# Performance work log

Hardware: AMD Instinct MI355X
Metric: run time of the kernel (lower is better)

## Reference

```python
import jax, jax.numpy as jnp
import numpy as np

CLB, CUB = 0.0, 255.0
SHORTCUT = (True, False, False, False, False)  # formatInput2Tuple((True,False), bool, 5, strict=False)


def _pad_same(kh, kw):
    kch, kcw = (kh + 1) // 2, (kw + 1) // 2
    return (kch - 1, kh - kch, kcw - 1, kw - kcw)


def _sym_pad(x, p):
    return jnp.pad(x, ((0, 0), (0, 0), (p[0], p[1]), (p[2], p[3])), mode='symmetric')


def _psf2otf(psf, shape):
    kh, kw = psf.shape[-2], psf.shape[-1]
    z = jnp.zeros(psf.shape[:-2] + shape, psf.dtype)
    z = z.at[..., :kh, :kw].set(psf)
    z = jnp.roll(z, (-(kh // 2), -(kw // 2)), axis=(-2, -1))
    return jnp.fft.fft2(z)


def _wnorm(w, scale):
    # zero-mean + L2 normalize per output filter, then learned per-filter scale
    wz = w - w.mean(axis=(-3, -2, -1), keepdims=True)
    n = jnp.sqrt((wz * wz).sum(axis=(-3, -2, -1), keepdims=True))
    return wz / n * scale[..., None, None, None]


def _conv2d(x, w, pad):
    return jax.lax.conv_general_dilated(_sym_pad(x, pad), w, (1, 1), 'VALID',
                                        dimension_numbers=('NCHW', 'OIHW', 'NCHW'))


def _convT2d(x, w, pad):
    # adjoint of VALID correlation, then crop by pad (nconv_transpose2D)
    kh, kw = w.shape[-2], w.shape[-1]
    wt = jnp.flip(w, (-2, -1)).transpose(1, 0, 2, 3)
    y = jax.lax.conv_general_dilated(x, wt, (1, 1), [(kh - 1, kh - 1), (kw - 1, kw - 1)],
                                     dimension_numbers=('NCHW', 'OIHW', 'NCHW'))
    return y[:, :, pad[0]:y.shape[2] - pad[1], pad[2]:y.shape[3] - pad[3]]


def _prelu(x, a):
    return jnp.where(x >= 0, x, a[None, :, None, None] * x)


def _edgetaper(x, psf):
    # MATLAB-style edgetaper: blend image with its circular blur near borders
    H, W = x.shape[-2], x.shape[-1]

    def a1(p, n):
        z = jnp.fft.ifft(jnp.abs(jnp.fft.fft(p, n - 1)) ** 2).real
        z = jnp.concatenate([z, z[:1]])
        return 1.0 - z / z.max()

    ah = a1(psf.sum(1), H)
    aw = a1(psf.sum(0), W)
    alpha = ah[:, None] * aw[None, :]
    otf = _psf2otf(psf, (H, W))
    blurred = jnp.fft.ifft2(jnp.fft.fft2(x) * otf[None, None]).real
    return alpha * x + (1.0 - alpha) * blurred


def _forward(x, blur_kernel, stdn, wiener_w, wiener_scale, alpha, conv_w, scale_f,
             bias_f, bias_t, rpa_prelu1, rpa_w1, rpa_scale1, rpa_b1,
             rpa_prelu2, rpa_w2, rpa_scale2, rpa_b2, alpha_proj, mix_weights):
    kh, kw = blur_kernel.shape
    pw = _pad_same(kh, kw)
    xp = _sym_pad(x, pw)
    xp = _edgetaper(xp, blur_kernel)
    B, C, Hp, Wp = xp.shape
    D = alpha.shape[0]

    # ---- multi-Wiener deconvolution in the Fourier domain ----
    ww = _wnorm(wiener_w, wiener_scale)                 # (F, wC, kh, kw)
    Hf = _psf2otf(blur_kernel, (Hp, Wp))                # (Hp, Wp) complex
    Gf = _psf2otf(ww, (Hp, Wp))                         # (F, wC, Hp, Wp)
    S = (jnp.abs(Gf) ** 2).sum(0)                       # (wC, Hp, Wp), wC=1 shared over channels
    Y = jnp.fft.fft2(xp)                                # (B, C, Hp, Wp)
    a = jnp.exp(alpha)                                  # (D, 1)
    denom = (jnp.abs(Hf) ** 2)[None, None] + a[:, :, None, None] * S[None]  # (D, C, Hp, Wp)
    T = jnp.conj(Hf)[None, None] / denom                # Wiener transfer functions
    xw = jnp.fft.ifft2(T[None] * Y[:, None]).real       # (B, D, C, Hp, Wp)
    amp = (jnp.abs(T) ** 2).mean(axis=(-2, -1))         # (D, C) noise amplification
    cstdn = jnp.sqrt(stdn[:, None] ** 2 * amp.mean(-1)[None])  # (B, D)
    cstdn = cstdn.reshape(-1)                           # (B*D,)

    z = xw.reshape(B * D, C, Hp, Wp)

    # ---- feature conv + residual pre-activation stack ----
    pc = _pad_same(conv_w.shape[-2], conv_w.shape[-1])
    cw = _wnorm(conv_w, scale_f)
    out = _conv2d(z, cw, pc) + bias_f[None, :, None, None]

    pr = _pad_same(rpa_w1.shape[-2], rpa_w1.shape[-1])
    for i in range(rpa_w1.shape[0]):
        t = _prelu(out, rpa_prelu1[i])
        t = _conv2d(t, _wnorm(rpa_w1[i], rpa_scale1[i]), pr) + rpa_b1[i][None, :, None, None]
        t = _prelu(t, rpa_prelu2[i])
        t = _conv2d(t, _wnorm(rpa_w2[i], rpa_scale2[i]), pr) + rpa_b2[i][None, :, None, None]
        out = out + t if SHORTCUT[i] else t

    out = _convT2d(out, cw, pc) + bias_t[None, :, None, None]

    # ---- L2 ball projection ----
    N = C * Hp * Wp
    eps = jnp.exp(alpha_proj[0]) * cstdn * np.float32(np.sqrt(N - 1))
    nrm = jnp.sqrt((out * out).sum(axis=(1, 2, 3)))
    scl = jnp.where(nrm > eps, eps / jnp.maximum(nrm, 1e-12), 1.0)
    out = out * scl[:, None, None, None]

    # ---- residual, box projection, crop, weighted mix over Wiener branches ----
    res = jnp.clip(z - out, CLB, CUB)
    res = res[:, :, pw[0]:Hp - pw[1], pw[2]:Wp - pw[3]]
    res = res.reshape(B, D, C, res.shape[-2], res.shape[-1])
    return (res * mix_weights).sum(axis=1)


def setup_inputs():
    key = jax.random.key(0)
    ks = jax.random.split(key, 8)
    B, C, H, W = 2, 1, 256, 256
    Dp = 5
    x = jax.random.uniform(ks[0], (B, C, H, W), jnp.float32) * 255.0
    bk = jax.random.uniform(ks[1], (15, 15), jnp.float32) + 1e-3
    bk = bk / bk.sum()
    stdn = jax.random.uniform(ks[2], (B,), jnp.float32) * 9.0 + 1.0
    return {
        'x': x,
        'blur_kernel': bk,
        'stdn': stdn,
        'wiener_w': jax.random.normal(ks[3], (24, 1, 5, 5), jnp.float32),
        'wiener_scale': jnp.full((24,), 0.1, jnp.float32),
        'alpha': jnp.log(jnp.logspace(np.log10(1e-3), np.log10(0.1), 4))[:, None].astype(jnp.float32),
        'conv_w': jax.random.normal(ks[4], (32, 1, 5, 5), jnp.float32),
        'scale_f': jnp.ones((32,), jnp.float32),
        'bias_f': jnp.zeros((32,), jnp.float32),
        'bias_t': jnp.zeros((1,), jnp.float32),
        'rpa_prelu1': jnp.full((Dp, 32), 0.1, jnp.float32),
        'rpa_w1': jax.random.normal(ks[5], (Dp, 64, 32, 3, 3), jnp.float32),
        'rpa_scale1': jnp.ones((Dp, 64), jnp.float32),
        'rpa_b1': jnp.zeros((Dp, 64), jnp.float32),
        'rpa_prelu2': jnp.full((Dp, 64), 0.1, jnp.float32),
        'rpa_w2': jax.random.normal(ks[6], (Dp, 32, 64, 3, 3), jnp.float32),
        'rpa_scale2': jnp.ones((Dp, 32), jnp.float32),
        'rpa_b2': jnp.zeros((Dp, 32), jnp.float32),
        'alpha_proj': jnp.zeros((1,), jnp.float32),
        'mix_weights': jnp.full((1, 4, 1, 1, 1), 0.25, jnp.float32),
    }


def reference(x, blur_kernel, stdn, wiener_w, wiener_scale, alpha, conv_w, scale_f,
              bias_f, bias_t, rpa_prelu1, rpa_w1, rpa_scale1, rpa_b1,
              rpa_prelu2, rpa_w2, rpa_scale2, rpa_b2, alpha_proj, mix_weights):
    return _forward(x, blur_kernel, stdn, wiener_w, wiener_scale, alpha, conv_w, scale_f,
                    bias_f, bias_t, rpa_prelu1, rpa_w1, rpa_scale1, rpa_b1,
                    rpa_prelu2, rpa_w2, rpa_scale2, rpa_b2, alpha_proj, mix_weights)
```

## Files before the change

### kernel.cpp

```cpp
#include <hip/hip_runtime.h>
#include <math.h>

#define HP     270
#define PLANE  72900
#define PW     272
#define PPLANE 73984

typedef unsigned int uint32;
typedef unsigned short ushort;
typedef __attribute__((ext_vector_type(8))) short bf16x8;
typedef __attribute__((ext_vector_type(4))) float f32x4;

__device__ __forceinline__ float blockReduceSum(float val) {
  __shared__ float sh[16];
  int lane = threadIdx.x & 63, wid = threadIdx.x >> 6;
#pragma unroll
  for (int o = 32; o > 0; o >>= 1) val += __shfl_down(val, o, 64);
  __syncthreads();
  if (lane == 0) sh[wid] = val;
  __syncthreads();
  float tot = 0.f;
  int nw = (blockDim.x + 63) >> 6;
  for (int i = 0; i < nw; ++i) tot += sh[i];
  return tot;
}

__global__ __launch_bounds__(256) void k_twiddle(float2* __restrict__ tw) {
  int idx = blockIdx.x * 256 + threadIdx.x;
  if (idx >= PLANE) return;
  int j = idx / HP, k = idx % HP;
  int m = (j * k) % HP;
  double ang = (2.0 * M_PI * (double)m) / 270.0;
  tw[idx] = make_float2((float)cos(ang), (float)sin(ang));
}

__global__ __launch_bounds__(256) void k_sympad(const float* __restrict__ x, float* __restrict__ xp) {
  int idx = blockIdx.x * 256 + threadIdx.x;
  if (idx >= 2 * PLANE) return;
  int b = idx / PLANE, p = idx % PLANE;
  int i = p / HP, j = p % HP;
  int si = i - 7; si = si < 0 ? -1 - si : (si > 255 ? 511 - si : si);
  int sj = j - 7; sj = sj < 0 ? -1 - sj : (sj > 255 ? 511 - sj : sj);
  xp[idx] = x[(b * 256 + si) * 256 + sj];
}

__global__ __launch_bounds__(512) void k_edget(const float* __restrict__ bk, float* __restrict__ ahw) {
  __shared__ float pr[15], pc[15], acr[15], accl[15];
  int t = threadIdx.x;
  if (t < 15) {
    float sr = 0.f, scv = 0.f;
    for (int k = 0; k < 15; ++k) { sr += bk[t * 15 + k]; scv += bk[k * 15 + t]; }
    pr[t] = sr; pc[t] = scv;
  }
  __syncthreads();
  if (t < 30) {
    int l = t % 15; bool isr = (t < 15);
    const float* p = isr ? pr : pc;
    float s = 0.f;
    for (int j = 0; j + l < 15; ++j) s += p[j] * p[j + l];
    if (isr) acr[l] = s; else accl[l] = s;
  }
  __syncthreads();
  for (int i = t; i < 540; i += blockDim.x) {
    bool isr = (i < 270);
    int ii = isr ? i : i - 270;
    const float* ac = isr ? acr : accl;
    int m = (ii == 269) ? 0 : ii;
    float zv;
    if (m < 15) zv = ac[m];
    else if (m >= 255) zv = ac[269 - m];
    else zv = 0.f;
    ahw[i] = 1.f - zv / ac[0];
  }
}

__global__ __launch_bounds__(256) void k_Hf(const float* __restrict__ bk, float2* __restrict__ Hf) {
  int p = blockIdx.x * 256 + threadIdx.x;
  if (p >= PLANE) return;
  int u = p / HP, v = p % HP;
  float2 er[15], es[15];
#pragma unroll
  for (int r = 0; r < 15; ++r) {
    int m = ((u * (r - 7)) % HP + HP) % HP;
    float sn, cs;
    sincosf(2.f * (float)M_PI * (float)m / 270.f, &sn, &cs);
    er[r] = make_float2(cs, -sn);
    int m2 = ((v * (r - 7)) % HP + HP) % HP;
    sincosf(2.f * (float)M_PI * (float)m2 / 270.f, &sn, &cs);
    es[r] = make_float2(cs, -sn);
  }
  float ar = 0.f, ai = 0.f;
#pragma unroll 1
  for (int r = 0; r < 15; ++r) {
    float rr = 0.f, ri = 0.f;
#pragma unroll
    for (int s = 0; s < 15; ++s) {
      float wv = bk[r * 15 + s];
      rr += wv * es[s].x; ri += wv * es[s].y;
    }
    ar += er[r].x * rr - er[r].y * ri;
    ai += er[r].x * ri + er[r].y * rr;
  }
  Hf[p] = make_float2(ar, ai);
}

__global__ __launch_bounds__(256) void k_wnorm(const float* __restrict__ w, const float* __restrict__ scale,
                                               float* __restrict__ out, int fsize) {
  int f = blockIdx.x;
  const float* wf = w + (size_t)f * fsize;
  float s = 0.f;
  for (int i = threadIdx.x; i < fsize; i += 256) s += wf[i];
  float mean = blockReduceSum(s) / (float)fsize;
  float s2 = 0.f;
  for (int i = threadIdx.x; i < fsize; i += 256) { float d = wf[i] - mean; s2 += d * d; }
  float nrm = sqrtf(blockReduceSum(s2));
  float sc = scale[f] / nrm;
  for (int i = threadIdx.x; i < fsize; i += 256) out[(size_t)f * fsize + i] = (wf[i] - mean) * sc;
}

__global__ void k_wT(const float* __restrict__ cwn, float* __restrict__ wT) {
  int idx = blockIdx.x * 256 + threadIdx.x;
  if (idx >= 800) return;
  int t = idx >> 5, f = idx & 31;
  int dri = t / 5, dci = t % 5;
  wT[t * 32 + f] = cwn[f * 25 + (4 - dri) * 5 + (4 - dci)];
}

template <int CIN, int COUT>
__global__ __launch_bounds__(256) void k_wfrag(const float* __restrict__ w, const float* __restrict__ scale,
                                               unsigned short* __restrict__ outb) {
  constexpr int KC = CIN / 32, MT = COUT / 16, FS = CIN * 9;
  int fg = blockIdx.x;
  int f = fg % COUT, iter = fg / COUT;
  const float* wf = w + (size_t)fg * FS;
  float s = 0.f;
  for (int i = threadIdx.x; i < FS; i += 256) s += wf[i];
  float mean = blockReduceSum(s) / (float)FS;
  float s2 = 0.f;
  for (int i = threadIdx.x; i < FS; i += 256) { float d = wf[i] - mean; s2 += d * d; }
  float nrm = sqrtf(blockReduceSum(s2));
  float scv = scale[fg] / nrm;
  unsigned short* dst0 = outb + (size_t)iter * (9 * KC * MT * 64 * 16);
  for (int i = threadIdx.x; i < FS; i += 256) {
    float val = (wf[i] - mean) * scv;
    int ci = i / 9, rs = i - ci * 9;
    int kc = ci >> 5, cil = ci & 31, q = cil >> 3, j = cil & 7;
    int mt = f >> 4, ocl = f & 15, lane = q * 16 + ocl;
    unsigned short* d2 = dst0 + ((((rs * KC + kc) * MT + mt) * 64 + lane) * 16);
    uint32 u = __float_as_uint(val);
    d2[j] = (unsigned short)(u >> 16);
    float lof = val - __uint_as_float(u & 0xFFFF0000u);
    d2[8 + j] = (unsigned short)(__float_as_uint(lof) >> 16);
  }
}

__global__ __launch_bounds__(256) void k_S(const float* __restrict__ wwn, float* __restrict__ S) {
  int p = blockIdx.x * 256 + threadIdx.x;
  if (p >= PLANE) return;
  int u = p / HP, v = p % HP;
  float2 er[5], es[5];
#pragma unroll
  for (int r = 0; r < 5; ++r) {
    float sn, cs;
    int m = (u * r) % HP;
    sincosf(2.f * (float)M_PI * (float)m / 270.f, &sn, &cs);
    er[r] = make_float2(cs, -sn);
    int m2 = (v * r) % HP;
    sincosf(2.f * (float)M_PI * (float)m2 / 270.f, &sn, &cs);
    es[r] = make_float2(cs, -sn);
  }
  float prr[25], pii[25];
#pragma unroll
  for (int r = 0; r < 5; ++r)
#pragma unroll
    for (int s = 0; s < 5; ++s) {
      prr[r * 5 + s] = er[r].x * es[s].x - er[r].y * es[s].y;
      pii[r * 5 + s] = er[r].x * es[s].y + er[r].y * es[s].x;
    }
  float acc = 0.f;
#pragma unroll 1
  for (int f = 0; f < 24; ++f) {
    float xr = 0.f, xi = 0.f;
#pragma unroll
    for (int t = 0; t < 25; ++t) {
      float wv = wwn[f * 25 + t];
      xr += wv * prr[t]; xi += wv * pii[t];
    }
    acc += xr * xr + xi * xi;
  }
  S[p] = acc;
}

__global__ __launch_bounds__(256) void k_T(const float2* __restrict__ Hf, const float* __restrict__ S,
                                           const float* __restrict__ alpha, float2* __restrict__ T) {
  int idx = blockIdx.x * 256 + threadIdx.x;
  if (idx >= 4 * PLANE) return;
  int d = idx / PLANE, p = idx % PLANE;
  float a = expf(alpha[d]);
  float2 h = Hf[p];
  float den = h.x * h.x + h.y * h.y + a * S[p];
  T[idx] = make_float2(h.x / den, -h.y / den);
}

__global__ __launch_bounds__(256) void k_amp(const float2* __restrict__ T, float* __restrict__ red) {
  int d = blockIdx.x;
  const float2* Td = T + (size_t)d * PLANE;
  float acc = 0.f;
  for (int i = threadIdx.x; i < PLANE; i += 256) { float2 t = Td[i]; acc += t.x * t.x + t.y * t.y; }
  float tot = blockReduceSum(acc);
  if (threadIdx.x == 0) red[d] = tot / (float)PLANE;
}

__global__ void k_eps(const float* __restrict__ apj, const float* __restrict__ stdn, float* __restrict__ red) {
  int s = threadIdx.x;
  if (s < 8) {
    int b = s >> 2, d = s & 3;
    red[8 + s] = expf(apj[0]) * stdn[b] * sqrtf(red[d]) * sqrtf(72899.f);
  }
}

__global__ void k_inv(const float* __restrict__ p, float* __restrict__ inv) {
  int t = threadIdx.x;
  if (t < 32) inv[t] = 1.f / p[t];
}

template <int NR, bool REALIN>
__global__ __launch_bounds__(64) void k_rowT(const void* __restrict__ inv_, float2* __restrict__ out,
                                             const float2* __restrict__ tw, float sgn) {
  int v = blockIdx.x * 64 + threadIdx.x;
  int r0 = blockIdx.y * NR;
  int m = blockIdx.z;
  bool ok = v < HP;
  int vc = ok ? v : 0;
  float P[NR], R[NR], Q[NR], Sm[NR];
#pragma unroll
  for (int i = 0; i < NR; ++i) { P[i] = R[i] = 0.f; if (!REALIN) { Q[i] = Sm[i] = 0.f; } }
  const float*  inR = (const float*)inv_  + ((size_t)m * HP + r0) * HP;
  const float2* inC = (const float2*)inv_ + ((size_t)m * HP + r0) * HP;
#pragma unroll 3
  for (int w = 0; w < HP; ++w) {
    float2 t = tw[w * HP + vc];
#pragma unroll
    for (int i = 0; i < NR; ++i) {
      if (REALIN) {
        float a = inR[i * HP + w];
        P[i] += a * t.x; R[i] += a * t.y;
      } else {
        float2 g = inC[i * HP + w];
        P[i] += g.x * t.x; Q[i] += g.y * t.y;
        R[i] += g.x * t.y; Sm[i] += g.y * t.x;
      }
    }
  }
  if (ok) {
#pragma unroll
    for (int i = 0; i < NR; ++i) {
      float ar, ai;
      if (REALIN) { ar = P[i]; ai = sgn * R[i]; }
      else        { ar = P[i] - sgn * Q[i]; ai = sgn * R[i] + Sm[i]; }
      out[((size_t)m * HP + r0 + i) * HP + v] = make_float2(ar, ai);
    }
  }
}

template <int NU, bool REALOUT>
__global__ __launch_bounds__(64) void k_colT(const float2* __restrict__ in, void* __restrict__ outv,
                                             const float2* __restrict__ tw, float sgn, float scale) {
  int v = blockIdx.x * 64 + threadIdx.x;
  int u0 = blockIdx.y * NU;
  int m = blockIdx.z;
  bool ok = v < HP;
  int vc = ok ? v : 0;
  float P[NU], Q[NU], R[NU], Sm[NU];
#pragma unroll
  for (int j = 0; j < NU; ++j) { P[j] = Q[j] = 0.f; if (!REALOUT) { R[j] = Sm[j] = 0.f; } }
  const float2* cp = in + (size_t)m * PLANE + vc;
#pragma unroll 3
  for (int h = 0; h < HP; ++h) {
    float2 g = cp[(size_t)h * HP];
    const float2* tr = tw + h * HP + u0;
#pragma unroll
    for (int j = 0; j < NU; ++j) {
      float2 t = tr[j];
      P[j] += g.x * t.x; Q[j] += g.y * t.y;
      if (!REALOUT) { R[j] += g.x * t.y; Sm[j] += g.y * t.x; }
    }
  }
  if (ok) {
#pragma unroll
    for (int j = 0; j < NU; ++j) {
      float ar = (P[j] - sgn * Q[j]) * scale;
      if (REALOUT) ((float*)outv)[((size_t)m * HP + u0 + j) * HP + v] = ar;
      else {
        float ai = (sgn * R[j] + Sm[j]) * scale;
        ((float2*)outv)[((size_t)m * HP + u0 + j) * HP + v] = make_float2(ar, ai);
      }
    }
  }
}

__global__ __launch_bounds__(256) void k_mulHf(const float2* __restrict__ in, const float2* __restrict__ Hf,
                                               float2* __restrict__ out) {
  int idx = blockIdx.x * 256 + threadIdx.x;
  if (idx >= 2 * PLANE) return;
  int p = idx % PLANE;
  float2 a = in[idx], b = Hf[p];
  out[idx] = make_float2(a.x * b.x - a.y * b.y, a.x * b.y + a.y * b.x);
}

__global__ __launch_bounds__(256) void k_taper(float* __restrict__ xp, const float* __restrict__ blr,
                                               const float* __restrict__ ahw) {
  int idx = blockIdx.x * 256 + threadIdx.x;
  if (idx >= 2 * PLANE) return;
  int p = idx % PLANE;
  int i = p / HP, j = p % HP;
  float al = ahw[i] * ahw[270 + j];
  xp[idx] = al * xp[idx] + (1.f - al) * blr[idx];
}

__global__ __launch_bounds__(256) void k_mulTY(const float2* __restrict__ T, const float2* __restrict__ Y,
                                               float2* __restrict__ out) {
  int idx = blockIdx.x * 256 + threadIdx.x;
  if (idx >= 8 * PLANE) return;
  int s = idx / PLANE, p = idx % PLANE;
  int b = s >> 2, d = s & 3;
  float2 a = T[(size_t)d * PLANE + p], y = Y[(size_t)b * PLANE + p];
  out[idx] = make_float2(a.x * y.x - a.y * y.y, a.x * y.y + a.y * y.x);
}

__device__ __forceinline__ uint32 rne_pack(float a, float b) {
  uint32 ua = __float_as_uint(a), ub = __float_as_uint(b);
  ua += 0x7FFFu + ((ua >> 16) & 1u);
  ub += 0x7FFFu + ((ub >> 16) & 1u);
  return (ua >> 16) | (ub & 0xFFFF0000u);
}

__device__ __forceinline__ ushort rne1(float a) {
  uint32 ua = __float_as_uint(a);
  ua += 0x7FFFu + ((ua >> 16) & 1u);
  return (ushort)(ua >> 16);
}

template <typename T, int STRIDE>
__device__ __forceinline__ void store_halo_s(T* __restrict__ op, int xx, int yy, int o, T val) {
  op[o] = val;
  bool xl = (xx == 0), xr = (xx == 269), yt = (yy == 0), yb = (yy == 269);
  if (xl) op[o - STRIDE] = val;
  if (xr) op[o + STRIDE] = val;
  if (yt) { op[o - PW * STRIDE] = val; if (xl) op[o - (PW + 1) * STRIDE] = val; if (xr) op[o - (PW - 1) * STRIDE] = val; }
  if (yb) { op[o + PW * STRIDE] = val; if (xl) op[o + (PW - 1) * STRIDE] = val; if (xr) op[o + (PW + 1) * STRIDE] = val; }
}

__global__ __launch_bounds__(256) void k_conv5(const float* __restrict__ z, const float* __restrict__ cw,
                                               const float* __restrict__ bias, const float* __restrict__ pre,
                                               uint4* __restrict__ actout) {
  int p = blockIdx.x * 256 + threadIdx.x;
  if (p >= PLANE) return;
  int sc = blockIdx.y;
  int i = p / HP, j = p % HP;
  const float* zs = z + (size_t)sc * PLANE;
  float v[25];
#pragma unroll
  for (int r = 0; r < 5; ++r) {
    int ii = i + r - 2; ii = ii < 0 ? -1 - ii : (ii > 269 ? 539 - ii : ii);
#pragma unroll
    for (int s = 0; s < 5; ++s) {
      int jj = j + s - 2; jj = jj < 0 ? -1 - jj : (jj > 269 ? 539 - jj : jj);
      v[r * 5 + s] = zs[ii * HP + jj];
    }
  }
  int o = (i + 1) * PW + (j + 1);
#pragma unroll 1
  for (int g = 0; g < 4; ++g) {
    float tt[8];
#pragma unroll
    for (int r8 = 0; r8 < 8; ++r8) {
      int oc = 8 * g + r8;
      float a = bias[oc];
#pragma unroll
      for (int k = 0; k < 25; ++k) a += cw[oc * 25 + k] * v[k];
      float pa = pre[oc];
      tt[r8] = fmaxf(a, 0.f) + pa * fminf(a, 0.f);
    }
    uint4 sp = make_uint4(rne_pack(tt[0], tt[1]), rne_pack(tt[2], tt[3]),
                          rne_pack(tt[4], tt[5]), rne_pack(tt[6], tt[7]));
    uint4* opb = actout + (size_t)(sc * 4 + g) * PPLANE;
    store_halo_s<uint4, 1>(opb, j, i, o, sp);
  }
}

#define TSTRIDE 144
template <int CIN, int COUT, bool SC, int OMODE>
__global__ __launch_bounds__(256, 3) void k_mconv(
    const uint4* __restrict__ act, const unsigned short* __restrict__ wf,
    const float* __restrict__ bias, const float* __restrict__ pre,
    uint2* __restrict__ actout, ushort* __restrict__ sout,
    const uint2* __restrict__ scact, const float* __restrict__ scinv,
    const float* __restrict__ wTt) {
  constexpr int KC = CIN / 32, MT = COUT / 16;
  __shared__ uint4 smem4[18 * 18 * TSTRIDE / 16];
  unsigned char* smem = (unsigned char*)smem4;

  const int lane = threadIdx.x & 63, wv = threadIdx.x >> 6;
  const int quad = lane >> 4, col = lane & 15;
  const int sc = blockIdx.y;
  int bx = blockIdx.x;
  int tile = (bx < 288) ? ((bx & 7) * 36 + (bx >> 3)) : 288;
  const int tx0 = (tile % 17) * 16, ty0 = (tile / 17) * 16;

  uint32 py[4], px[4], boff[4];
  bool vld[4];
#pragma unroll
  for (int nt = 0; nt < 4; ++nt) {
    int xr = tx0 + col, yr = ty0 + wv * 4 + nt;
    vld[nt] = (xr < 270) && (yr < 270);
    int xx = xr > 269 ? 269 : xr;
    int yy = yr > 269 ? 269 : yr;
    px[nt] = xx; py[nt] = yy;
    boff[nt] = (yy + 1) * PW + xx;
  }

  f32x4 acc[MT][4];
#pragma unroll
  for (int mt = 0; mt < MT; ++mt)
#pragma unroll
    for (int nt = 0; nt < 4; ++nt) { f32x4 z = {0.f, 0.f, 0.f, 0.f}; acc[mt][nt] = z; }

  {
    const uint4* srcb = act + (size_t)(sc * (CIN / 8)) * PPLANE;
    for (int i = threadIdx.x; i < 324 * (CIN / 8); i += 256) {
      int g = i / 324, pxl = i - g * 324;
      int pyy = pxl / 18, pxx = pxl - pyy * 18;
      int gy = ty0 + pyy; if (gy > 271) gy = 271;
      int gx = tx0 + pxx; if (gx > 271) gx = 271;
      uint4 v = srcb[(size_t)g * PPLANE + gy * PW + gx];
      *(uint4*)(smem + pxl * TSTRIDE + g * 16) = v;
    }
  }
  __syncthreads();
#pragma unroll 1
  for (int kc = 0; kc < KC; ++kc) {
#pragma unroll
    for (int o = 0; o < 9; ++o) {
      const int dy = o / 3, dx = o % 3;
      union { uint4 u; bf16x8 v; } Wh[MT], Wl[MT];
#pragma unroll
      for (int mt = 0; mt < MT; ++mt) {
        const uint4* wp = (const uint4*)wf + ((((o * KC + kc) * MT + mt) * 64 + lane) * 2);
        Wh[mt].u = wp[0]; Wl[mt].u = wp[1];
      }
      const int lx = col + dx;
#pragma unroll
      for (int nt = 0; nt < 4; ++nt) {
        const int ly = wv * 4 + nt + dy;
        union { uint4 u; bf16x8 v; } B;
        B.u = *(const uint4*)(smem + (ly * 18 + lx) * TSTRIDE + (kc * 4 + quad) * 16);
#pragma unroll
        for (int mt = 0; mt < MT; ++mt)
          acc[mt][nt] = __builtin_amdgcn_mfma_f32_16x16x32_bf16(Wh[mt].v, B.v, acc[mt][nt], 0, 0, 0);
#pragma unroll
        for (int mt = 0; mt < MT; ++mt)
          acc[mt][nt] = __builtin_amdgcn_mfma_f32_16x16x32_bf16(Wl[mt].v, B.v, acc[mt][nt], 0, 0, 0);
      }
    }
  }

  if (OMODE == 1) {
#pragma unroll
    for (int mt = 0; mt < MT; ++mt) {
      const int ocb = mt * 16 + quad * 4;
      const int g2 = 2 * mt + (quad >> 1), slot = quad & 1;
      f32x4 bias4 = *(const f32x4*)(bias + ocb);
      f32x4 pr4 = *(const f32x4*)(pre + ocb);
      f32x4 inv4;
      if (SC) inv4 = *(const f32x4*)(scinv + ocb);
#pragma unroll
      for (int nt = 0; nt < 4; ++nt) {
        if (!vld[nt]) continue;
        const uint32 ppix = boff[nt] + 1;
        float v0 = acc[mt][nt][0] + bias4[0], v1 = acc[mt][nt][1] + bias4[1];
        float v2 = acc[mt][nt][2] + bias4[2], v3 = acc[mt][nt][3] + bias4[3];
        if (SC) {
          uint2 h = scact[((size_t)(sc * (COUT / 8) + g2) * PPLANE + ppix) * 2 + slot];
          float s0 = __uint_as_float(h.x << 16), s1 = __uint_as_float(h.x & 0xFFFF0000u);
          float s2 = __uint_as_float(h.y << 16), s3 = __uint_as_float(h.y & 0xFFFF0000u);
          v0 += (s0 >= 0.f) ? s0 : s0 * inv4[0];
          v1 += (s1 >= 0.f) ? s1 : s1 * inv4[1];
          v2 += (s2 >= 0.f) ? s2 : s2 * inv4[2];
          v3 += (s3 >= 0.f) ? s3 : s3 * inv4[3];
        }
        float t0 = fmaxf(v0, 0.f) + pr4[0] * fminf(v0, 0.f);
        float t1 = fmaxf(v1, 0.f) + pr4[1] * fminf(v1, 0.f);
        float t2 = fmaxf(v2, 0.f) + pr4[2] * fminf(v2, 0.f);
        float t3 = fmaxf(v3, 0.f) + pr4[3] * fminf(v3, 0.f);
        uint2 sp = make_uint2(rne_pack(t0, t1), rne_pack(t2, t3));
        uint2* opb = actout + (size_t)(sc * (COUT / 8) + g2) * PPLANE * 2;
        store_halo_s<uint2, 2>(opb, (int)px[nt], (int)py[nt], (int)ppix * 2 + slot, sp);
      }
    }
  } else {
    float4 b4[MT];
#pragma unroll
    for (int mt = 0; mt < MT; ++mt) b4[mt] = *(const float4*)(bias + mt * 16 + quad * 4);
#pragma unroll
    for (int nt = 0; nt < 4; ++nt) {
      float vv[MT][4];
#pragma unroll
      for (int mt = 0; mt < MT; ++mt) {
        vv[mt][0] = acc[mt][nt][0] + b4[mt].x;
        vv[mt][1] = acc[mt][nt][1] + b4[mt].y;
        vv[mt][2] = acc[mt][nt][2] + b4[mt].z;
        vv[mt][3] = acc[mt][nt][3] + b4[mt].w;
      }
      ushort* sp = sout + (size_t)sc * 25 * PLANE + (int)(py[nt] * 270 + px[nt]);
#pragma unroll
      for (int t = 0; t < 25; ++t) {
        const float* wp = wTt + t * 32 + quad * 4;
        float c = 0.f;
#pragma unroll
        for (int mt = 0; mt < MT; ++mt) {
          float4 w4 = *(const float4*)(wp + mt * 16);
          c += w4.x * vv[mt][0] + w4.y * vv[mt][1] + w4.z * vv[mt][2] + w4.w * vv[mt][3];
        }
        c += __shfl_xor(c, 16, 64);
        c += __shfl_xor(c, 32, 64);
        if (quad == 0 && vld[nt]) sp[(size_t)t * PLANE] = rne1(c);
      }
    }
  }
}

__global__ __launch_bounds__(256) void k_convT2(const ushort* __restrict__ s, const float* __restrict__ bt,
                                                float* __restrict__ yo) {
  int p = blockIdx.x * 256 + threadIdx.x;
  if (p >= PLANE) return;
  int sc = blockIdx.y;
  int y = p / 270, x = p - y * 270;
  float acc = bt[0];
  const ushort* sb = s + (size_t)sc * 25 * PLANE;
#pragma unroll
  for (int a = 0; a < 5; ++a) {
    int yy = y + a - 2;
    if ((unsigned)yy >= 270u) continue;
    const ushort* row = sb + (size_t)(a * 5) * PLANE + yy * 270;
#pragma unroll
    for (int b = 0; b < 5; ++b) {
      int xx = x + b - 2;
      if ((unsigned)xx < 270u) acc += __uint_as_float(((uint32)row[(size_t)b * PLANE + xx]) << 16);
    }
  }
  yo[(size_t)sc * PLANE + p] = acc;
}

__global__ __launch_bounds__(256) void k_nrm(const float* __restrict__ yb, float* __restrict__ red) {
  int s = blockIdx.x;
  const float* ys = yb + (size_t)s * PLANE;
  float acc = 0.f;
  for (int i = threadIdx.x; i < PLANE; i += 256) { float v = ys[i]; acc += v * v; }
  float tot = blockReduceSum(acc);
  if (threadIdx.x == 0) {
    float nrm = sqrtf(tot);
    float eps = red[8 + s];
    red[16 + s] = (nrm > eps) ? eps / fmaxf(nrm, 1e-12f) : 1.0f;
  }
}

__global__ __launch_bounds__(256) void k_final(const float* __restrict__ z, const float* __restrict__ yb,
                                               const float* __restrict__ red, const float* __restrict__ mw,
                                               float* __restrict__ out) {
  int idx = blockIdx.x * 256 + threadIdx.x;
  if (idx >= 131072) return;
  int b = idx >> 16;
  int rem = idx & 65535;
  int h = rem >> 8, w = rem & 255;
  int p = (h + 7) * HP + (w + 7);
  float acc = 0.f;
#pragma unroll
  for (int d = 0; d < 4; ++d) {
    int s = b * 4 + d;
    float v = z[(size_t)s * PLANE + p] - red[16 + s] * yb[(size_t)s * PLANE + p];
    v = fminf(fmaxf(v, 0.f), 255.f);
    acc += mw[d] * v;
  }
  out[idx] = acc;
}

extern "C" void kernel_launch(void* const* d_in, const int* in_sizes, int n_in,
                              void* d_out, int out_size, void* d_ws, size_t ws_size,
                              hipStream_t stream) {
  (void)in_sizes; (void)n_in; (void)out_size;
  const float* x    = (const float*)d_in[0];
  const float* bk   = (const float*)d_in[1];
  const float* stdn = (const float*)d_in[2];
  const float* ww   = (const float*)d_in[3];
  const float* wwsc = (const float*)d_in[4];
  const float* alph = (const float*)d_in[5];
  const float* cw   = (const float*)d_in[6];
  const float* sf   = (const float*)d_in[7];
  const float* bf   = (const float*)d_in[8];
  const float* bt   = (const float*)d_in[9];
  const float* p1   = (const float*)d_in[10];
  const float* w1   = (const float*)d_in[11];
  const float* s1   = (const float*)d_in[12];
  const float* b1   = (const float*)d_in[13];
  const float* p2   = (const float*)d_in[14];
  const float* w2   = (const float*)d_in[15];
  const float* s2   = (const float*)d_in[16];
  const float* b2   = (const float*)d_in[17];
  const float* apj  = (const float*)d_in[18];
  const float* mwp  = (const float*)d_in[19];
  float* out = (float*)d_out;

  char* wsbase = (char*)d_ws;
  size_t off = 0;
  auto alloc = [&](size_t nbytes) -> char* {
    char* p = wsbase + off;
    off = (off + nbytes + 255) & ~(size_t)255;
    return p;
  };
  float*  zb  = (float*)alloc(8 * (size_t)PLANE * 4);
  float*  yb  = (float*)alloc(8 * (size_t)PLANE * 4);
  float*  red = (float*)alloc(64 * 4);
  float*  inv = (float*)alloc(32 * 4);
  float*  cwn = (float*)alloc(800 * 4);
  float*  wTt = (float*)alloc(800 * 4);
  unsigned short* w1f = (unsigned short*)alloc(5 * 36864 * (size_t)2);
  unsigned short* w2f = (unsigned short*)alloc(5 * 36864 * (size_t)2);
  size_t U0 = off;
  float2* tw  = (float2*)alloc(2 * (size_t)PLANE * 4);
  float*  xp  = (float*)alloc(2 * (size_t)PLANE * 4);
  float*  rtm = (float*)alloc(2 * (size_t)PLANE * 4);
  float2* cb0 = (float2*)alloc(2 * 8 * (size_t)PLANE * 8);
  float2* cb1 = (float2*)alloc(2 * 8 * (size_t)PLANE * 8);
  float2* Yb  = (float2*)alloc(2 * 2 * (size_t)PLANE * 8);
  float2* Hf  = (float2*)alloc(2 * (size_t)PLANE * 4);
  float*  Sb  = (float*)alloc((size_t)PLANE * 4);
  float2* Tb  = (float2*)alloc(2 * 4 * (size_t)PLANE * 4);
  float*  ahw = (float*)alloc(540 * 4);
  float*  wwn = (float*)alloc(600 * 4);
  size_t conv8 = (size_t)8 * 4 * PPLANE * 16 + 256 + (size_t)8 * 8 * PPLANE * 16 + 256;
  int S = (ws_size >= U0 + conv8) ? 8 : 4;
  int nc = 8 / S;
  off = U0;
  uint4* act1 = (uint4*)alloc((size_t)S * 4 * PPLANE * 16);
  uint4* act2 = (uint4*)alloc((size_t)S * 8 * PPLANE * 16);
  ushort* sOb = (ushort*)act1;

  k_twiddle<<<285, 256, 0, stream>>>(tw);
  k_sympad<<<(2 * PLANE + 255) / 256, 256, 0, stream>>>(x, xp);
  k_edget<<<1, 512, 0, stream>>>(bk, ahw);
  k_Hf<<<285, 256, 0, stream>>>(bk, Hf);
  k_wnorm<<<24, 256, 0, stream>>>(ww, wwsc, wwn, 25);
  k_wnorm<<<32, 256, 0, stream>>>(cw, sf, cwn, 25);
  k_wT<<<4, 256, 0, stream>>>(cwn, wTt);
  k_wfrag<32, 64><<<320, 256, 0, stream>>>(w1, s1, w1f);
  k_wfrag<64, 32><<<160, 256, 0, stream>>>(w2, s2, w2f);
  k_inv<<<1, 32, 0, stream>>>(p1, inv);
  k_S<<<285, 256, 0, stream>>>(wwn, Sb);
  k_T<<<(4 * PLANE + 255) / 256, 256, 0, stream>>>(Hf, Sb, alph, Tb);
  k_amp<<<4, 256, 0, stream>>>(Tb, red);
  k_eps<<<1, 64, 0, stream>>>(apj, stdn, red);

  dim3 g2(5, 45, 2), g8(5, 45, 8);

  k_rowT<6, true ><<<g2, 64, 0, stream>>>(xp, cb1, tw, -1.f);
  k_colT<6, false><<<g2, 64, 0, stream>>>(cb1, cb0, tw, -1.f, 1.f);
  k_mulHf<<<(2 * PLANE + 255) / 256, 256, 0, stream>>>(cb0, Hf, cb1);
  k_rowT<6, false><<<g2, 64, 0, stream>>>(cb1, cb0, tw, 1.f);
  k_colT<6, true ><<<g2, 64, 0, stream>>>(cb0, rtm, tw, 1.f, 1.f / (float)PLANE);
  k_taper<<<(2 * PLANE + 255) / 256, 256, 0, stream>>>(xp, rtm, ahw);

  k_rowT<6, true ><<<g2, 64, 0, stream>>>(xp, cb1, tw, -1.f);
  k_colT<6, false><<<g2, 64, 0, stream>>>(cb1, Yb, tw, -1.f, 1.f);

  k_mulTY<<<(8 * PLANE + 255) / 256, 256, 0, stream>>>(Tb, Yb, cb0);
  k_rowT<6, false><<<g8, 64, 0, stream>>>(cb0, cb1, tw, 1.f);
  k_colT<6, true ><<<g8, 64, 0, stream>>>(cb1, zb, tw, 1.f, 1.f / (float)PLANE);

  for (int c = 0; c < nc; ++c) {
    const float* zc = zb + (size_t)c * S * PLANE;
    float* ybc = yb + (size_t)c * S * PLANE;
    k_conv5<<<dim3(285, S), 256, 0, stream>>>(zc, cwn, bf, p1, act1);
    for (int i = 0; i < 5; ++i) {
      k_mconv<32, 64, false, 1><<<dim3(289, S), 256, 0, stream>>>(
          act1, w1f + (size_t)i * 36864, b1 + i * 64, p2 + i * 64, (uint2*)act2, nullptr, nullptr, nullptr, nullptr);
      if (i == 0)
        k_mconv<64, 32, true, 1><<<dim3(289, S), 256, 0, stream>>>(
            act2, w2f + (size_t)i * 36864, b2 + i * 32, p1 + (i + 1) * 32, (uint2*)act1, nullptr, (const uint2*)act1, inv, nullptr);
      else if (i < 4)
        k_mconv<64, 32, false, 1><<<dim3(289, S), 256, 0, stream>>>(
            act2, w2f + (size_t)i * 36864, b2 + i * 32, p1 + (i + 1) * 32, (uint2*)act1, nullptr, nullptr, nullptr, nullptr);
      else
        k_mconv<64, 32, false, 2><<<dim3(289, S), 256, 0, stream>>>(
            act2, w2f + (size_t)i * 36864, b2 + i * 32, nullptr, nullptr, sOb, nullptr, nullptr, wTt);
    }
    k_convT2<<<dim3(285, S), 256, 0, stream>>>(sOb, bt, ybc);
  }

  k_nrm<<<8, 256, 0, stream>>>(yb, red);
  k_final<<<(131072 + 255) / 256, 256, 0, stream>>>(zb, yb, red, mwp, out);
}
```

Baseline: 1.348 ms.

## Fuse paired 3x3 residual convs into one kernel with LDS-resident intermediate

Each residual block's two 3x3 bf16 MFMA convolutions (32->64 and 64->32) now run in one kernel. The first conv is computed over an 18x18 halo region from a 20x20 input tile, and its 64-channel result is kept in shared memory for the second conv. This removes the global write and read of the 64-channel intermediate and halves the kernel launches. In exchange the first conv is recomputed on halo pixels, and shared memory rises to about 78KB per block, so launch bounds drop to 2 blocks per CU. Activations now ping-pong between two 32-channel buffers.

Result: faster. 1.199 ms (-11.1%).

```diff
diff --git a/kernel.cpp b/kernel.cpp
--- a/kernel.cpp
+++ b/kernel.cpp
@@ -389,17 +389,18 @@
   }
 }
 
-#define TSTRIDE 144
-template <int CIN, int COUT, bool SC, int OMODE>
-__global__ __launch_bounds__(256, 3) void k_mconv(
-    const uint4* __restrict__ act, const unsigned short* __restrict__ wf,
-    const float* __restrict__ bias, const float* __restrict__ pre,
+template <bool SC, int OMODE>
+__global__ __launch_bounds__(256, 2) void k_fused(
+    const uint4* __restrict__ actin, const unsigned short* __restrict__ w1fb,
+    const unsigned short* __restrict__ w2fb,
+    const float* __restrict__ b1v, const float* __restrict__ p2v,
+    const float* __restrict__ b2v, const float* __restrict__ p1v,
     uint2* __restrict__ actout, ushort* __restrict__ sout,
     const uint2* __restrict__ scact, const float* __restrict__ scinv,
     const float* __restrict__ wTt) {
-  constexpr int KC = CIN / 32, MT = COUT / 16;
-  __shared__ uint4 smem4[18 * 18 * TSTRIDE / 16];
-  unsigned char* smem = (unsigned char*)smem4;
+  __shared__ uint4 smemAll[(32000 + 46656) / 16];
+  unsigned char* st0 = (unsigned char*)smemAll;
+  unsigned char* st1 = (unsigned char*)smemAll + 32000;
 
   const int lane = threadIdx.x & 63, wv = threadIdx.x >> 6;
   const int quad = lane >> 4, col = lane & 15;
@@ -407,6 +408,78 @@
   int bx = blockIdx.x;
   int tile = (bx < 288) ? ((bx & 7) * 36 + (bx >> 3)) : 288;
   const int tx0 = (tile % 17) * 16, ty0 = (tile / 17) * 16;
+
+  {
+    const uint4* srcb = actin + (size_t)(sc * 4) * PPLANE;
+    for (int i = threadIdx.x; i < 1600; i += 256) {
+      int g = i / 400, pxl = i - g * 400;
+      int ry = pxl / 20, rx = pxl - ry * 20;
+      int pr = ty0 - 1 + ry; pr = pr < 0 ? 0 : (pr > 271 ? 271 : pr);
+      int pc = tx0 - 1 + rx; pc = pc < 0 ? 0 : (pc > 271 ? 271 : pc);
+      uint4 v = srcb[(size_t)g * PPLANE + pr * PW + pc];
+      *(uint4*)(st0 + pxl * 80 + g * 16) = v;
+    }
+  }
+  __syncthreads();
+
+  {
+    int rb[6], pcl6[6];
+#pragma unroll
+    for (int s = 0; s < 6; ++s) {
+      int p = (wv * 6 + s) * 16 + col; if (p > 323) p = 323;
+      pcl6[s] = p;
+      int iy = p / 18, ix = p - iy * 18;
+      int gy = ty0 - 1 + iy; gy = gy < 0 ? 0 : (gy > 269 ? 269 : gy);
+      int gx = tx0 - 1 + ix; gx = gx < 0 ? 0 : (gx > 269 ? 269 : gx);
+      rb[s] = (((gy - ty0 + 1) * 20) + (gx - tx0 + 1)) * 80 + quad * 16;
+    }
+    f32x4 a1[4][6];
+#pragma unroll
+    for (int mt = 0; mt < 4; ++mt)
+#pragma unroll
+      for (int s = 0; s < 6; ++s) { f32x4 z = {0.f, 0.f, 0.f, 0.f}; a1[mt][s] = z; }
+#pragma unroll
+    for (int o = 0; o < 9; ++o) {
+      const int dy = o / 3, dx = o % 3;
+      const int doff = (dy * 20 + dx) * 80;
+      union { uint4 u; bf16x8 v; } Wh[4], Wl[4];
+#pragma unroll
+      for (int mt = 0; mt < 4; ++mt) {
+        const uint4* wp = (const uint4*)w1fb + (((o * 4 + mt) * 64 + lane) * 2);
+        Wh[mt].u = wp[0]; Wl[mt].u = wp[1];
+      }
+#pragma unroll
+      for (int s = 0; s < 6; ++s) {
+        union { uint4 u; bf16x8 v; } B;
+        B.u = *(const uint4*)(st0 + rb[s] + doff);
+#pragma unroll
+        for (int mt = 0; mt < 4; ++mt)
+          a1[mt][s] = __builtin_amdgcn_mfma_f32_16x16x32_bf16(Wh[mt].v, B.v, a1[mt][s], 0, 0, 0);
+#pragma unroll
+        for (int mt = 0; mt < 4; ++mt)
+          a1[mt][s] = __builtin_amdgcn_mfma_f32_16x16x32_bf16(Wl[mt].v, B.v, a1[mt][s], 0, 0, 0);
+      }
+    }
+#pragma unroll
+    for (int mt = 0; mt < 4; ++mt) {
+      const int ocb = mt * 16 + quad * 4;
+      const int g2 = 2 * mt + (quad >> 1), slot = quad & 1;
+      f32x4 b4 = *(const f32x4*)(b1v + ocb);
+      f32x4 pr4 = *(const f32x4*)(p2v + ocb);
+#pragma unroll
+      for (int s = 0; s < 6; ++s) {
+        float v0 = a1[mt][s][0] + b4[0], v1 = a1[mt][s][1] + b4[1];
+        float v2 = a1[mt][s][2] + b4[2], v3 = a1[mt][s][3] + b4[3];
+        float t0 = fmaxf(v0, 0.f) + pr4[0] * fminf(v0, 0.f);
+        float t1 = fmaxf(v1, 0.f) + pr4[1] * fminf(v1, 0.f);
+        float t2 = fmaxf(v2, 0.f) + pr4[2] * fminf(v2, 0.f);
+        float t3 = fmaxf(v3, 0.f) + pr4[3] * fminf(v3, 0.f);
+        uint2 sp = make_uint2(rne_pack(t0, t1), rne_pack(t2, t3));
+        *(uint2*)(st1 + pcl6[s] * 144 + g2 * 16 + slot * 8) = sp;
+      }
+    }
+  }
+  __syncthreads();
 
   uint32 py[4], px[4], boff[4];
   bool vld[4];
@@ -419,34 +492,20 @@
     px[nt] = xx; py[nt] = yy;
     boff[nt] = (yy + 1) * PW + xx;
   }
-
-  f32x4 acc[MT][4];
-#pragma unroll
-  for (int mt = 0; mt < MT; ++mt)
+  f32x4 acc[2][4];
+#pragma unroll
+  for (int mt = 0; mt < 2; ++mt)
 #pragma unroll
     for (int nt = 0; nt < 4; ++nt) { f32x4 z = {0.f, 0.f, 0.f, 0.f}; acc[mt][nt] = z; }
-
-  {
-    const uint4* srcb = act + (size_t)(sc * (CIN / 8)) * PPLANE;
-    for (int i = threadIdx.x; i < 324 * (CIN / 8); i += 256) {
-      int g = i / 324, pxl = i - g * 324;
-      int pyy = pxl / 18, pxx = pxl - pyy * 18;
-      int gy = ty0 + pyy; if (gy > 271) gy = 271;
-      int gx = tx0 + pxx; if (gx > 271) gx = 271;
-      uint4 v = srcb[(size_t)g * PPLANE + gy * PW + gx];
-      *(uint4*)(smem + pxl * TSTRIDE + g * 16) = v;
-    }
-  }
-  __syncthreads();
 #pragma unroll 1
-  for (int kc = 0; kc < KC; ++kc) {
+  for (int kc = 0; kc < 2; ++kc) {
 #pragma unroll
     for (int o = 0; o < 9; ++o) {
       const int dy = o / 3, dx = o % 3;
-      union { uint4 u; bf16x8 v; } Wh[MT], Wl[MT];
-#pragma unroll
-      for (int mt = 0; mt < MT; ++mt) {
-        const uint4* wp = (const uint4*)wf + ((((o * KC + kc) * MT + mt) * 64 + lane) * 2);
+      union { uint4 u; bf16x8 v; } Wh[2], Wl[2];
+#pragma unroll
+      for (int mt = 0; mt < 2; ++mt) {
+        const uint4* wp = (const uint4*)w2fb + ((((o * 2 + kc) * 2 + mt) * 64 + lane) * 2);
         Wh[mt].u = wp[0]; Wl[mt].u = wp[1];
       }
       const int lx = col + dx;
@@ -454,12 +513,12 @@
       for (int nt = 0; nt < 4; ++nt) {
         const int ly = wv * 4 + nt + dy;
         union { uint4 u; bf16x8 v; } B;
-        B.u = *(const uint4*)(smem + (ly * 18 + lx) * TSTRIDE + (kc * 4 + quad) * 16);
-#pragma unroll
-        for (int mt = 0; mt < MT; ++mt)
+        B.u = *(const uint4*)(st1 + (ly * 18 + lx) * 144 + (kc * 4 + quad) * 16);
+#pragma unroll
+        for (int mt = 0; mt < 2; ++mt)
           acc[mt][nt] = __builtin_amdgcn_mfma_f32_16x16x32_bf16(Wh[mt].v, B.v, acc[mt][nt], 0, 0, 0);
 #pragma unroll
-        for (int mt = 0; mt < MT; ++mt)
+        for (int mt = 0; mt < 2; ++mt)
           acc[mt][nt] = __builtin_amdgcn_mfma_f32_16x16x32_bf16(Wl[mt].v, B.v, acc[mt][nt], 0, 0, 0);
       }
     }
@@ -467,11 +526,11 @@
 
   if (OMODE == 1) {
 #pragma unroll
-    for (int mt = 0; mt < MT; ++mt) {
+    for (int mt = 0; mt < 2; ++mt) {
       const int ocb = mt * 16 + quad * 4;
       const int g2 = 2 * mt + (quad >> 1), slot = quad & 1;
-      f32x4 bias4 = *(const f32x4*)(bias + ocb);
-      f32x4 pr4 = *(const f32x4*)(pre + ocb);
+      f32x4 bias4 = *(const f32x4*)(b2v + ocb);
+      f32x4 pr4 = *(const f32x4*)(p1v + ocb);
       f32x4 inv4;
       if (SC) inv4 = *(const f32x4*)(scinv + ocb);
 #pragma unroll
@@ -481,7 +540,7 @@
         float v0 = acc[mt][nt][0] + bias4[0], v1 = acc[mt][nt][1] + bias4[1];
         float v2 = acc[mt][nt][2] + bias4[2], v3 = acc[mt][nt][3] + bias4[3];
         if (SC) {
-          uint2 h = scact[((size_t)(sc * (COUT / 8) + g2) * PPLANE + ppix) * 2 + slot];
+          uint2 h = scact[((size_t)(sc * 4 + g2) * PPLANE + ppix) * 2 + slot];
           float s0 = __uint_as_float(h.x << 16), s1 = __uint_as_float(h.x & 0xFFFF0000u);
           float s2 = __uint_as_float(h.y << 16), s3 = __uint_as_float(h.y & 0xFFFF0000u);
           v0 += (s0 >= 0.f) ? s0 : s0 * inv4[0];
@@ -494,19 +553,19 @@
         float t2 = fmaxf(v2, 0.f) + pr4[2] * fminf(v2, 0.f);
         float t3 = fmaxf(v3, 0.f) + pr4[3] * fminf(v3, 0.f);
         uint2 sp = make_uint2(rne_pack(t0, t1), rne_pack(t2, t3));
-        uint2* opb = actout + (size_t)(sc * (COUT / 8) + g2) * PPLANE * 2;
+        uint2* opb = actout + (size_t)(sc * 4 + g2) * PPLANE * 2;
         store_halo_s<uint2, 2>(opb, (int)px[nt], (int)py[nt], (int)ppix * 2 + slot, sp);
       }
     }
   } else {
-    float4 b4[MT];
-#pragma unroll
-    for (int mt = 0; mt < MT; ++mt) b4[mt] = *(const float4*)(bias + mt * 16 + quad * 4);
+    float4 b4[2];
+#pragma unroll
+    for (int mt = 0; mt < 2; ++mt) b4[mt] = *(const float4*)(b2v + mt * 16 + quad * 4);
 #pragma unroll
     for (int nt = 0; nt < 4; ++nt) {
-      float vv[MT][4];
-#pragma unroll
-      for (int mt = 0; mt < MT; ++mt) {
+      float vv[2][4];
+#pragma unroll
+      for (int mt = 0; mt < 2; ++mt) {
         vv[mt][0] = acc[mt][nt][0] + b4[mt].x;
         vv[mt][1] = acc[mt][nt][1] + b4[mt].y;
         vv[mt][2] = acc[mt][nt][2] + b4[mt].z;
@@ -518,7 +577,7 @@
         const float* wp = wTt + t * 32 + quad * 4;
         float c = 0.f;
 #pragma unroll
-        for (int mt = 0; mt < MT; ++mt) {
+        for (int mt = 0; mt < 2; ++mt) {
           float4 w4 = *(const float4*)(wp + mt * 16);
           c += w4.x * vv[mt][0] + w4.y * vv[mt][1] + w4.z * vv[mt][2] + w4.w * vv[mt][3];
         }
@@ -638,13 +697,13 @@
   float2* Tb  = (float2*)alloc(2 * 4 * (size_t)PLANE * 4);
   float*  ahw = (float*)alloc(540 * 4);
   float*  wwn = (float*)alloc(600 * 4);
-  size_t conv8 = (size_t)8 * 4 * PPLANE * 16 + 256 + (size_t)8 * 8 * PPLANE * 16 + 256;
+  size_t conv8 = 2 * ((size_t)8 * 4 * PPLANE * 16 + 256);
   int S = (ws_size >= U0 + conv8) ? 8 : 4;
   int nc = 8 / S;
   off = U0;
-  uint4* act1 = (uint4*)alloc((size_t)S * 4 * PPLANE * 16);
-  uint4* act2 = (uint4*)alloc((size_t)S * 8 * PPLANE * 16);
-  ushort* sOb = (ushort*)act1;
+  uint4* actA = (uint4*)alloc((size_t)S * 4 * PPLANE * 16);
+  uint4* actB = (uint4*)alloc((size_t)S * 4 * PPLANE * 16);
+  ushort* sOb = (ushort*)actB;
 
   k_twiddle<<<285, 256, 0, stream>>>(tw);
   k_sympad<<<(2 * PLANE + 255) / 256, 256, 0, stream>>>(x, xp);
@@ -680,20 +739,17 @@
   for (int c = 0; c < nc; ++c) {
     const float* zc = zb + (size_t)c * S * PLANE;
     float* ybc = yb + (size_t)c * S * PLANE;
-    k_conv5<<<dim3(285, S), 256, 0, stream>>>(zc, cwn, bf, p1, act1);
-    for (int i = 0; i < 5; ++i) {
-      k_mconv<32, 64, false, 1><<<dim3(289, S), 256, 0, stream>>>(
-          act1, w1f + (size_t)i * 36864, b1 + i * 64, p2 + i * 64, (uint2*)act2, nullptr, nullptr, nullptr, nullptr);
-      if (i == 0)
-        k_mconv<64, 32, true, 1><<<dim3(289, S), 256, 0, stream>>>(
-            act2, w2f + (size_t)i * 36864, b2 + i * 32, p1 + (i + 1) * 32, (uint2*)act1, nullptr, (const uint2*)act1, inv, nullptr);
-      else if (i < 4)
-        k_mconv<64, 32, false, 1><<<dim3(289, S), 256, 0, stream>>>(
-            act2, w2f + (size_t)i * 36864, b2 + i * 32, p1 + (i + 1) * 32, (uint2*)act1, nullptr, nullptr, nullptr, nullptr);
-      else
-        k_mconv<64, 32, false, 2><<<dim3(289, S), 256, 0, stream>>>(
-            act2, w2f + (size_t)i * 36864, b2 + i * 32, nullptr, nullptr, sOb, nullptr, nullptr, wTt);
-    }
+    k_conv5<<<dim3(285, S), 256, 0, stream>>>(zc, cwn, bf, p1, actA);
+    k_fused<true, 1><<<dim3(289, S), 256, 0, stream>>>(
+        actA, w1f, w2f, b1, p2, b2, p1 + 32, (uint2*)actB, nullptr, (const uint2*)actA, inv, nullptr);
+    k_fused<false, 1><<<dim3(289, S), 256, 0, stream>>>(
+        actB, w1f + 36864, w2f + 36864, b1 + 64, p2 + 64, b2 + 32, p1 + 64, (uint2*)actA, nullptr, nullptr, nullptr, nullptr);
+    k_fused<false, 1><<<dim3(289, S), 256, 0, stream>>>(
+        actA, w1f + 2 * 36864, w2f + 2 * 36864, b1 + 128, p2 + 128, b2 + 64, p1 + 96, (uint2*)actB, nullptr, nullptr, nullptr, nullptr);
+    k_fused<false, 1><<<dim3(289, S), 256, 0, stream>>>(
+        actB, w1f + 3 * 36864, w2f + 3 * 36864, b1 + 192, p2 + 192, b2 + 96, p1 + 128, (uint2*)actA, nullptr, nullptr, nullptr, nullptr);
+    k_fused<false, 2><<<dim3(289, S), 256, 0, stream>>>(
+        actA, w1f + 4 * 36864, w2f + 4 * 36864, b1 + 256, p2 + 256, b2 + 128, nullptr, nullptr, sOb, nullptr, nullptr, wTt);
     k_convT2<<<dim3(285, S), 256, 0, stream>>>(sOb, bt, ybc);
   }
 
```
